# Optimization experiments

Hardware: AMD Instinct MI355X
Metric: run time of the kernel (lower is better)

The kernel has to match this reference:

```python
import jax, jax.numpy as jnp
import numpy as np

B, T, D = 1, 2048, 1024
H = 16
HD = D // H
K = 4
FF = 4 * D
LAYERS = 24
EPS = 1.1920929e-07  # torch.finfo(float32).eps, RMSNorm default


def setup_inputs() -> dict:
    key = jax.random.key(0)
    ks = jax.random.split(key, 16)
    s = 0.02
    return {
        "x": jax.random.normal(ks[0], (B, T, D), jnp.float32),
        "gamma": jax.random.uniform(ks[1], (D,), jnp.float32),
        "beta": jax.random.normal(ks[2], (D,), jnp.float32) * 0.1,
        "iter_scale": jax.random.uniform(ks[3], (1,), jnp.float32),
        "qkv_bases": jax.random.normal(ks[4], (K, 3 * D, D), jnp.float32) * s,
        "o_bases": jax.random.normal(ks[5], (K, D, D), jnp.float32) * s,
        "gate_bases": jax.random.normal(ks[6], (K, FF, D), jnp.float32) * s,
        "up_bases": jax.random.normal(ks[7], (K, FF, D), jnp.float32) * s,
        "down_bases": jax.random.normal(ks[8], (K, D, FF), jnp.float32) * s,
        "alpha_qkv": jax.random.normal(ks[9], (LAYERS, K), jnp.float32) * 0.1 + jnp.eye(LAYERS, K)[:, :K] * 0.0 + jnp.concatenate([jnp.ones((LAYERS, 1)), jnp.zeros((LAYERS, K - 1))], axis=1),
        "alpha_o": jnp.concatenate([jnp.ones((LAYERS, 1)), jnp.zeros((LAYERS, K - 1))], axis=1) + jax.random.normal(ks[10], (LAYERS, K)) * 0.1,
        "alpha_gate": jnp.concatenate([jnp.ones((LAYERS, 1)), jnp.zeros((LAYERS, K - 1))], axis=1) + jax.random.normal(ks[11], (LAYERS, K)) * 0.1,
        "alpha_up": jnp.concatenate([jnp.ones((LAYERS, 1)), jnp.zeros((LAYERS, K - 1))], axis=1) + jax.random.normal(ks[12], (LAYERS, K)) * 0.1,
        "alpha_down": jnp.concatenate([jnp.ones((LAYERS, 1)), jnp.zeros((LAYERS, K - 1))], axis=1) + jax.random.normal(ks[13], (LAYERS, K)) * 0.1,
        "norm1_w": jnp.ones((D,), jnp.float32),
        "norm2_w": jnp.ones((D,), jnp.float32),
        "layer_idx": 5,
    }


def _rmsnorm(x, w):
    return x * jax.lax.rsqrt(jnp.mean(x * x, axis=-1, keepdims=True) + EPS) * w


def reference(x, gamma, beta, iter_scale, qkv_bases, o_bases, gate_bases, up_bases,
              down_bases, alpha_qkv, alpha_o, alpha_gate, alpha_up, alpha_down,
              norm1_w, norm2_w, layer_idx):
    Bx, Tx, Dx = x.shape
    # --- attention sub-block ---
    h = _rmsnorm(x, norm1_w) * gamma + beta
    W_qkv = jnp.einsum('k,kij->ij', alpha_qkv[layer_idx], qkv_bases)  # [3D, D]
    qkv = jnp.einsum('btd,od->bto', h, W_qkv).reshape(Bx, Tx, 3, H, HD)
    qkv = jnp.transpose(qkv, (2, 0, 3, 1, 4))  # [3, B, H, T, HD]
    q, k, v = qkv[0], qkv[1], qkv[2]
    scores = jnp.einsum('bhqd,bhkd->bhqk', q, k) / jnp.sqrt(jnp.asarray(HD, x.dtype))
    causal = jnp.tril(jnp.ones((Tx, Tx), bool))
    scores = jnp.where(causal, scores, jnp.asarray(-jnp.inf, scores.dtype))
    attn = jax.nn.softmax(scores, axis=-1)
    out = jnp.einsum('bhqk,bhkd->bhqd', attn, v)
    out = jnp.transpose(out, (0, 2, 1, 3)).reshape(Bx, Tx, Dx)
    W_o = jnp.einsum('k,kij->ij', alpha_o[layer_idx], o_bases)
    x_attn = x + jnp.einsum('btd,od->bto', out, W_o)
    # --- SwiGLU FFN sub-block ---
    h2 = _rmsnorm(x_attn, norm2_w) * gamma + beta
    W_g = jnp.einsum('k,kij->ij', alpha_gate[layer_idx], gate_bases)
    W_u = jnp.einsum('k,kij->ij', alpha_up[layer_idx], up_bases)
    W_d = jnp.einsum('k,kij->ij', alpha_down[layer_idx], down_bases)
    gate = jnp.einsum('btd,fd->btf', h2, W_g)
    up = jnp.einsum('btd,fd->btf', h2, W_u)
    ffn_out = jnp.einsum('btf,df->btd', jax.nn.silu(gate) * up, W_d)
    block_out = x_attn + ffn_out
    return x + (block_out - x) * iter_scale
```

## Files before the change

### kernel.cpp

```cpp
#include <hip/hip_runtime.h>
#include <hip/hip_bf16.h>
#include <math.h>

typedef __bf16 bf16;
typedef __bf16 bf16x8 __attribute__((ext_vector_type(8)));
typedef __bf16 bf16x4 __attribute__((ext_vector_type(4)));
typedef float f32x4 __attribute__((ext_vector_type(4)));

#define EPSc 1.1920929e-07f
#define LOG2E 1.44269504f

static __device__ __forceinline__ void glds16(const void* g, void* l) {
  __builtin_amdgcn_global_load_lds((const __attribute__((address_space(1))) void*)g,
                                   (__attribute__((address_space(3))) void*)l, 16, 0, 0);
}

static __device__ __forceinline__ bf16x4 comb4(const float* b0, const float* b1,
                                               const float* b2, const float* b3,
                                               float a0, float a1, float a2, float a3) {
  float4 v0 = *(const float4*)b0, v1 = *(const float4*)b1;
  float4 v2 = *(const float4*)b2, v3 = *(const float4*)b3;
  bf16x4 o;
  o[0] = (bf16)(a0*v0.x + a1*v1.x + a2*v2.x + a3*v3.x);
  o[1] = (bf16)(a0*v0.y + a1*v1.y + a2*v2.y + a3*v3.y);
  o[2] = (bf16)(a0*v0.z + a1*v1.z + a2*v2.z + a3*v3.z);
  o[3] = (bf16)(a0*v0.w + a1*v1.w + a2*v2.w + a3*v3.w);
  return o;
}

__global__ __launch_bounds__(256)
void prep1(const float* __restrict__ qkv_b, const float* __restrict__ a_qkv,
           const float* __restrict__ o_b,   const float* __restrict__ a_o,
           const float* __restrict__ x, const float* __restrict__ n1w,
           const float* __restrict__ gamma, const float* __restrict__ beta,
           const int* __restrict__ lidx,
           bf16* __restrict__ Wqkv, bf16* __restrict__ Wo, bf16* __restrict__ hbuf) {
  const int bid = blockIdx.x, tid = threadIdx.x;
  if (bid < 4096) {
    int li = lidx[0];
    const float* base; const float* al; bf16* out; size_t flat, n;
    if (bid < 3072) { base = qkv_b; al = a_qkv; out = Wqkv; flat = (size_t)bid << 10; n = (size_t)3072*1024; }
    else            { base = o_b;   al = a_o;   out = Wo;   flat = (size_t)(bid-3072) << 10; n = (size_t)1024*1024; }
    float a0 = al[li*4], a1 = al[li*4+1], a2 = al[li*4+2], a3 = al[li*4+3];
    size_t off = flat + tid*4;
    bf16x4 o = comb4(base+off, base+n+off, base+2*n+off, base+3*n+off, a0, a1, a2, a3);
    *(bf16x4*)&out[off] = o;
  } else {
    int row = bid - 4096, t = tid;
    const float4* xr = (const float4*)(x + (size_t)row*1024);
    float4 v = xr[t];
    float ss = v.x*v.x + v.y*v.y + v.z*v.z + v.w*v.w;
    #pragma unroll
    for (int off = 32; off > 0; off >>= 1) ss += __shfl_down(ss, off, 64);
    __shared__ float red[4];
    if ((t & 63) == 0) red[t >> 6] = ss;
    __syncthreads();
    float tot = red[0] + red[1] + red[2] + red[3];
    float r = rsqrtf(tot * (1.0f/1024.0f) + EPSc);
    float4 wv = ((const float4*)n1w)[t];
    float4 gv = ((const float4*)gamma)[t];
    float4 bv = ((const float4*)beta)[t];
    bf16x4 o;
    o[0] = (bf16)(v.x*r*wv.x*gv.x + bv.x);
    o[1] = (bf16)(v.y*r*wv.y*gv.y + bv.y);
    o[2] = (bf16)(v.z*r*wv.z*gv.z + bv.z);
    o[3] = (bf16)(v.w*r*wv.w*gv.w + bv.w);
    *(bf16x4*)&hbuf[(size_t)row*1024 + t*4] = o;
  }
}

__global__ __launch_bounds__(256) void rmsnorm_k(const float* __restrict__ x,
                                                 const float* __restrict__ w,
                                                 const float* __restrict__ gamma,
                                                 const float* __restrict__ beta,
                                                 bf16* __restrict__ out) {
  int row = blockIdx.x, t = threadIdx.x;
  const float4* xr = (const float4*)(x + (size_t)row*1024);
  float4 v = xr[t];
  float ss = v.x*v.x + v.y*v.y + v.z*v.z + v.w*v.w;
  #pragma unroll
  for (int off = 32; off > 0; off >>= 1) ss += __shfl_down(ss, off, 64);
  __shared__ float red[4];
  if ((t & 63) == 0) red[t >> 6] = ss;
  __syncthreads();
  float tot = red[0] + red[1] + red[2] + red[3];
  float r = rsqrtf(tot * (1.0f/1024.0f) + EPSc);
  float4 wv = ((const float4*)w)[t];
  float4 gv = ((const float4*)gamma)[t];
  float4 bv = ((const float4*)beta)[t];
  bf16x4 o;
  o[0] = (bf16)(v.x*r*wv.x*gv.x + bv.x);
  o[1] = (bf16)(v.y*r*wv.y*gv.y + bv.y);
  o[2] = (bf16)(v.z*r*wv.z*gv.z + bv.z);
  o[3] = (bf16)(v.w*r*wv.w*gv.w + bv.w);
  *(bf16x4*)&out[(size_t)row*1024 + t*4] = o;
}

template<int EP, int NTW>
__global__ __launch_bounds__(256)
void gemm_bt(const bf16* __restrict__ A, const bf16* __restrict__ Bw,
             int M, int N, int K, int lda, int ldb, int gx,
             float* __restrict__ outf, bf16* __restrict__ outb,
             const float* __restrict__ auxf, const float* __restrict__ auxf2,
             const float* __restrict__ iscale) {
  constexpr int BN = NTW * 32;
  __shared__ __align__(16) bf16 As[2][128*64];
  __shared__ __align__(16) bf16 Bs[2][BN*64];
  const int nwg = gridDim.x;
  const int orig = blockIdx.x;
  const int wg = (orig & 7) * (nwg >> 3) + (orig >> 3);
  const int tn0 = (wg % gx) * BN, tm0 = (wg / gx) * 128;
  const int tid = threadIdx.x, wave = tid >> 6, lane = tid & 63;
  const int lr = lane & 15, lg = lane >> 4;
  const int wr = wave >> 1, wc = wave & 1;
  f32x4 acc[4][NTW] = {};
  const int rs = lane >> 3, cs = (lane & 7) * 8;

  const bf16* Abase = A + (size_t)tm0 * lda;
  const bf16* Bbase = Bw + (size_t)tn0 * ldb;

  auto stage = [&](bf16* as, bf16* bs, int k0) {
    #pragma unroll
    for (int j = 0; j < 4; ++j) {
      int chunk = wave*4 + j;
      int r = chunk*8 + rs;
      glds16(Abase + (size_t)r*lda + k0 + cs, as + chunk*512 + lane*8);
    }
    #pragma unroll
    for (int j = 0; j < NTW; ++j) {
      int chunk = wave*NTW + j;
      int r = chunk*8 + rs;
      glds16(Bbase + (size_t)r*ldb + k0 + cs, bs + chunk*512 + lane*8);
    }
  };
  auto comp = [&](const bf16* as, const bf16* bs) {
    #pragma unroll
    for (int kk = 0; kk < 2; ++kk) {
      bf16x8 av[4], bv[NTW];
      #pragma unroll
      for (int m = 0; m < 4; ++m) av[m] = *(const bf16x8*)&as[(wr*64 + m*16 + lr)*64 + kk*32 + lg*8];
      #pragma unroll
      for (int n = 0; n < NTW; ++n) bv[n] = *(const bf16x8*)&bs[(wc*NTW*16 + n*16 + lr)*64 + kk*32 + lg*8];
      #pragma unroll
      for (int m = 0; m < 4; ++m)
        #pragma unroll
        for (int n = 0; n < NTW; ++n)
          acc[m][n] = __builtin_amdgcn_mfma_f32_16x16x32_bf16(av[m], bv[n], acc[m][n], 0, 0, 0);
    }
  };

  bf16 *a0 = As[0], *a1 = As[1], *b0 = Bs[0], *b1 = Bs[1];
  stage(a0, b0, 0);
  __syncthreads();
  for (int k0 = 64; k0 < K; k0 += 64) {
    stage(a1, b1, k0);
    comp(a0, b0);
    __syncthreads();
    bf16* t;
    t = a0; a0 = a1; a1 = t;
    t = b0; b0 = b1; b1 = t;
  }
  comp(a0, b0);

  float its = 0.f;
  if constexpr (EP == 4) its = iscale[0];

  if constexpr (EP == 5) {
    #pragma unroll
    for (int m = 0; m < 4; ++m)
      #pragma unroll
      for (int j = 0; j < NTW/2; ++j)
        #pragma unroll
        for (int i = 0; i < 4; ++i) {
          int row = tm0 + wr*64 + m*16 + lg*4 + i;
          int col = (tn0 >> 1) + wc*(NTW*8) + j*16 + lr;
          float g = acc[m][2*j][i], u = acc[m][2*j+1][i];
          float s = g / (1.f + __builtin_amdgcn_exp2f(-g * LOG2E));
          outb[(size_t)row * (N >> 1) + col] = (bf16)(s * u);
        }
  } else {
    #pragma unroll
    for (int m = 0; m < 4; ++m)
      #pragma unroll
      for (int n = 0; n < NTW; ++n)
        #pragma unroll
        for (int i = 0; i < 4; ++i) {
          int row = tm0 + wr*64 + m*16 + lg*4 + i;
          int col = tn0 + wc*NTW*16 + n*16 + lr;
          size_t idx = (size_t)row * N + col;
          float v = acc[m][n][i];
          if constexpr (EP == 0) outb[idx] = (bf16)v;
          else if constexpr (EP == 1) outf[idx] = auxf[idx] + v;
          else if constexpr (EP == 4) {
            float xv = auxf[idx], xa = auxf2[idx];
            outf[idx] = xv + (xa + v - xv) * its;
          } else if constexpr (EP == 6) outf[idx] = v;
        }
  }
}

__global__ __launch_bounds__(256)
void reduce2(const float* __restrict__ p0, const float* __restrict__ p1,
             const float* __restrict__ x, const float* __restrict__ xat,
             const float* __restrict__ iscale, float* __restrict__ out) {
  size_t i = (size_t)blockIdx.x * 256 + threadIdx.x;
  float its = iscale[0];
  float4 a = ((const float4*)p0)[i], b = ((const float4*)p1)[i];
  float4 xv = ((const float4*)x)[i], xa = ((const float4*)xat)[i];
  float4 o;
  o.x = xv.x + (xa.x + a.x + b.x - xv.x) * its;
  o.y = xv.y + (xa.y + a.y + b.y - xv.y) * its;
  o.z = xv.z + (xa.z + a.z + b.z - xv.z) * its;
  o.w = xv.w + (xa.w + a.w + b.w - xv.w) * its;
  ((float4*)out)[i] = o;
}

__global__ __launch_bounds__(256)
void attn_mega(const bf16* __restrict__ qkv, bf16* __restrict__ out,
               const float* __restrict__ gate_b, const float* __restrict__ up_b,
               const float* __restrict__ down_b,
               const float* __restrict__ a_gate, const float* __restrict__ a_up,
               const float* __restrict__ a_down, const int* __restrict__ lidx,
               bf16* __restrict__ Wgu, bf16* __restrict__ Wd) {
  __shared__ __align__(16) bf16 Ks[2][64*72];
  __shared__ __align__(16) bf16 Vt[2][64*66];
  __shared__ __align__(16) bf16 Ps[4][16*68];
  const int bid = blockIdx.x;
  const int tid = threadIdx.x;

  if (bid < 256) {
    const int cb = bid;
    int li = lidx[0];
    float g0 = a_gate[li*4], g1 = a_gate[li*4+1], g2 = a_gate[li*4+2], g3 = a_gate[li*4+3];
    float u0 = a_up[li*4],   u1 = a_up[li*4+1],   u2 = a_up[li*4+2],   u3 = a_up[li*4+3];
    float d0 = a_down[li*4], d1 = a_down[li*4+1], d2 = a_down[li*4+2], d3 = a_down[li*4+3];
    const size_t PS = (size_t)4096 * 1024;
    for (int it = 0; it < 48; ++it) {
      int chunk = it * 256 + cb;
      if (chunk < 8192) {
        int r = chunk, w = r & 31;
        int f = ((r >> 5) << 4) + (w & 15);
        const float* base = (w < 16) ? gate_b : up_b;
        float a0 = (w < 16) ? g0 : u0, a1 = (w < 16) ? g1 : u1;
        float a2 = (w < 16) ? g2 : u2, a3 = (w < 16) ? g3 : u3;
        size_t src = (size_t)f*1024 + tid*4;
        bf16x4 o = comb4(base+src, base+PS+src, base+2*PS+src, base+3*PS+src, a0, a1, a2, a3);
        *(bf16x4*)&Wgu[((size_t)r << 10) + tid*4] = o;
      } else {
        size_t off = ((size_t)(chunk - 8192) << 10) + tid*4;
        bf16x4 o = comb4(down_b+off, down_b+PS+off, down_b+2*PS+off, down_b+3*PS+off, d0, d1, d2, d3);
        *(bf16x4*)&Wd[off] = o;
      }
    }
    return;
  }

  const int a = bid - 256;
  const int qb = 31 - (a >> 4);
  const int h = (a & 7) + 8 * ((a >> 3) & 1);
  const int wave = tid >> 6, lane = tid & 63;
  const int lr = lane & 15, lg = lane >> 4;
  const int q0 = qb * 64;

  bf16x8 qf[2];
  {
    const bf16* qrow = qkv + (size_t)(q0 + wave*16 + lr)*3072 + h*64;
    qf[0] = *(const bf16x8*)(qrow + lg*8);
    qf[1] = *(const bf16x8*)(qrow + 32 + lg*8);
  }
  f32x4 o[4] = {};
  float mrow[4], lrow[4];
  #pragma unroll
  for (int i = 0; i < 4; ++i) { mrow[i] = -__builtin_inff(); lrow[i] = 0.f; }

  const int r0 = tid >> 3, r1 = (tid + 256) >> 3;
  const int c0 = (tid & 7) << 3;
  const bf16* kb = qkv + 1024 + h*64 + c0;
  const bf16* vb = qkv + 2048 + h*64 + c0;

  bf16x8 kreg[2], vreg[2];
  auto stage_load = [&](int kv0) {
    kreg[0] = *(const bf16x8*)(kb + (size_t)(kv0 + r0)*3072);
    kreg[1] = *(const bf16x8*)(kb + (size_t)(kv0 + r1)*3072);
    vreg[0] = *(const bf16x8*)(vb + (size_t)(kv0 + r0)*3072);
    vreg[1] = *(const bf16x8*)(vb + (size_t)(kv0 + r1)*3072);
  };
  auto stage_write = [&](int buf) {
    *(bf16x8*)&Ks[buf][r0*72 + c0] = kreg[0];
    *(bf16x8*)&Ks[buf][r1*72 + c0] = kreg[1];
    #pragma unroll
    for (int e = 0; e < 8; ++e) Vt[buf][(c0 + e)*66 + r0] = vreg[0][e];
    #pragma unroll
    for (int e = 0; e < 8; ++e) Vt[buf][(c0 + e)*66 + r1] = vreg[1][e];
  };

  stage_load(0);
  stage_write(0);
  __syncthreads();
  int cur = 0;

  const float C = 0.125f * LOG2E;

  for (int t = 0; t <= qb; ++t) {
    const int kv0 = t * 64;
    if (t < qb) stage_load(kv0 + 64);

    f32x4 s[4] = {};
    __builtin_amdgcn_s_setprio(1);
    #pragma unroll
    for (int n = 0; n < 4; ++n) {
      bf16x8 k0f = *(const bf16x8*)&Ks[cur][(n*16 + lr)*72 + lg*8];
      s[n] = __builtin_amdgcn_mfma_f32_16x16x32_bf16(qf[0], k0f, s[n], 0, 0, 0);
      bf16x8 k1f = *(const bf16x8*)&Ks[cur][(n*16 + lr)*72 + 32 + lg*8];
      s[n] = __builtin_amdgcn_mfma_f32_16x16x32_bf16(qf[1], k1f, s[n], 0, 0, 0);
    }
    __builtin_amdgcn_s_setprio(0);

    if (t == qb) {
      const int qbase = q0 + wave*16 + lg*4;
      #pragma unroll
      for (int n = 0; n < 4; ++n)
        #pragma unroll
        for (int i = 0; i < 4; ++i)
          if (kv0 + n*16 + lr > qbase + i) s[n][i] = -__builtin_inff();
    }

    float mnewr[4], pmn[4];
    #pragma unroll
    for (int i = 0; i < 4; ++i) mnewr[i] = fmaxf(fmaxf(s[0][i], s[1][i]), fmaxf(s[2][i], s[3][i]));
    #pragma unroll
    for (int i = 0; i < 4; ++i)
      #pragma unroll
      for (int off = 1; off < 16; off <<= 1) mnewr[i] = fmaxf(mnewr[i], __shfl_xor(mnewr[i], off, 64));
    bool grow = false;
    #pragma unroll
    for (int i = 0; i < 4; ++i) { pmn[i] = mnewr[i] * C; grow = grow || (pmn[i] > mrow[i] + 8.f); }
    if (__any(grow)) {
      #pragma unroll
      for (int i = 0; i < 4; ++i) {
        float mt = fmaxf(mrow[i], pmn[i]);
        float fc = __builtin_amdgcn_exp2f(mrow[i] - mt);
        mrow[i] = mt;
        lrow[i] *= fc;
        #pragma unroll
        for (int nd = 0; nd < 4; ++nd) o[nd][i] *= fc;
      }
    }
    float rsum[4] = {0.f, 0.f, 0.f, 0.f};
    #pragma unroll
    for (int n = 0; n < 4; ++n)
      #pragma unroll
      for (int i = 0; i < 4; ++i) {
        float e = __builtin_amdgcn_exp2f(__builtin_fmaf(s[n][i], C, -mrow[i]));
        s[n][i] = e;
        rsum[i] += e;
      }
    #pragma unroll
    for (int i = 0; i < 4; ++i)
      #pragma unroll
      for (int off = 1; off < 16; off <<= 1) rsum[i] += __shfl_xor(rsum[i], off, 64);
    #pragma unroll
    for (int i = 0; i < 4; ++i) lrow[i] += rsum[i];
    #pragma unroll
    for (int n = 0; n < 4; ++n)
      #pragma unroll
      for (int i = 0; i < 4; ++i) Ps[wave][(lg*4 + i)*68 + n*16 + lr] = (bf16)s[n][i];
    asm volatile("s_waitcnt lgkmcnt(0)" ::: "memory");
    __builtin_amdgcn_s_setprio(1);
    #pragma unroll
    for (int kk = 0; kk < 2; ++kk) {
      bf16x8 pf = *(const bf16x8*)&Ps[wave][lr*68 + kk*32 + lg*8];
      #pragma unroll
      for (int nd = 0; nd < 4; ++nd) {
        bf16x8 vf = *(const bf16x8*)&Vt[cur][(nd*16 + lr)*66 + kk*32 + lg*8];
        o[nd] = __builtin_amdgcn_mfma_f32_16x16x32_bf16(pf, vf, o[nd], 0, 0, 0);
      }
    }
    __builtin_amdgcn_s_setprio(0);
    if (t < qb) {
      stage_write(cur ^ 1);
      __syncthreads();
      cur ^= 1;
    }
  }
  #pragma unroll
  for (int i = 0; i < 4; ++i) {
    float inv = 1.f / lrow[i];
    #pragma unroll
    for (int nd = 0; nd < 4; ++nd)
      out[(size_t)(q0 + wave*16 + lg*4 + i)*1024 + h*64 + nd*16 + lr] = (bf16)(o[nd][i]*inv);
  }
}

extern "C" void kernel_launch(void* const* d_in, const int* in_sizes, int n_in,
                              void* d_out, int out_size, void* d_ws, size_t ws_size,
                              hipStream_t stream) {
  const float* x        = (const float*)d_in[0];
  const float* gamma    = (const float*)d_in[1];
  const float* beta     = (const float*)d_in[2];
  const float* iscale   = (const float*)d_in[3];
  const float* qkv_b    = (const float*)d_in[4];
  const float* o_b      = (const float*)d_in[5];
  const float* gate_b   = (const float*)d_in[6];
  const float* up_b     = (const float*)d_in[7];
  const float* down_b   = (const float*)d_in[8];
  const float* a_qkv    = (const float*)d_in[9];
  const float* a_o      = (const float*)d_in[10];
  const float* a_gate   = (const float*)d_in[11];
  const float* a_up     = (const float*)d_in[12];
  const float* a_down   = (const float*)d_in[13];
  const float* n1w      = (const float*)d_in[14];
  const float* n2w      = (const float*)d_in[15];
  const int*   lidx     = (const int*)d_in[16];

  char* p = (char*)d_ws;
  auto alloc = [&](size_t bytes) { char* r = p; p += (bytes + 255) & ~(size_t)255; return r; };
  bf16*  Wqkv = (bf16*)alloc((size_t)3072*1024*2);
  bf16*  Wo   = (bf16*)alloc((size_t)1024*1024*2);
  bf16*  Wgu  = (bf16*)alloc((size_t)8192*1024*2);
  bf16*  Wd   = (bf16*)alloc((size_t)1024*4096*2);
  bf16*  hbuf = (bf16*)alloc((size_t)2048*1024*2);
  bf16*  qkvb = (bf16*)alloc((size_t)2048*3072*2);
  bf16*  attn = (bf16*)alloc((size_t)2048*1024*2);
  float* xat  = (float*)alloc((size_t)2048*1024*4);
  bf16*  h2   = (bf16*)alloc((size_t)2048*1024*2);
  bf16*  act  = (bf16*)alloc((size_t)2048*4096*2);
  float* out  = (float*)d_out;
  float* part0 = (float*)Wqkv;
  float* part1 = (float*)qkvb;

  prep1<<<6144, 256, 0, stream>>>(qkv_b, a_qkv, o_b, a_o, x, n1w, gamma, beta, lidx,
                                  Wqkv, Wo, hbuf);
  gemm_bt<0,4><<<24*16, 256, 0, stream>>>(hbuf, Wqkv, 2048, 3072, 1024, 1024, 1024, 24,
                                          nullptr, qkvb, nullptr, nullptr, nullptr);
  attn_mega<<<768, 256, 0, stream>>>(qkvb, attn, gate_b, up_b, down_b,
                                     a_gate, a_up, a_down, lidx, Wgu, Wd);
  gemm_bt<1,2><<<16*16, 256, 0, stream>>>(attn, Wo, 2048, 1024, 1024, 1024, 1024, 16,
                                          xat, nullptr, x, nullptr, nullptr);
  rmsnorm_k<<<2048, 256, 0, stream>>>(xat, n2w, gamma, beta, h2);
  gemm_bt<5,4><<<64*16, 256, 0, stream>>>(h2, Wgu, 2048, 8192, 1024, 1024, 1024, 64,
                                          nullptr, act, nullptr, nullptr, nullptr);
  gemm_bt<6,2><<<16*16, 256, 0, stream>>>(act, Wd, 2048, 1024, 2048, 4096, 4096, 16,
                                          part0, nullptr, nullptr, nullptr, nullptr);
  gemm_bt<6,2><<<16*16, 256, 0, stream>>>(act + 2048, Wd + 2048, 2048, 1024, 2048, 4096, 4096, 16,
                                          part1, nullptr, nullptr, nullptr, nullptr);
  reduce2<<<2048, 256, 0, stream>>>(part0, part1, x, xat, iscale, out);
}
```

Measured before the change: 234.9 us.

## Add 256x256 gate/up GEMM kernel, swizzle LDS, drop split-K down projection

Adds a dedicated 512-thread gate/up GEMM with 256x256 tiles and a finer-grained double-buffered pipeline that interleaves global-to-LDS staging with MFMA phases. It also puts an XOR swizzle on the LDS layout in the generic GEMM to cut bank conflicts. The down projection becomes one full-K GEMM with a fused residual/iter_scale epilogue, which removes the split-K partial buffers and the reduce kernel. The trade-off is that the down projection now runs only 256 workgroups over K=4096, giving less parallelism. The new gate/up kernel also hardcodes its shapes.

```diff
diff --git a/kernel.cpp b/kernel.cpp
--- a/kernel.cpp
+++ b/kernel.cpp
@@ -114,7 +114,10 @@
   const int lr = lane & 15, lg = lane >> 4;
   const int wr = wave >> 1, wc = wave & 1;
   f32x4 acc[4][NTW] = {};
-  const int rs = lane >> 3, cs = (lane & 7) * 8;
+  const int rs = lane >> 3;
+  const int sc = (((lane & 7) ^ rs) << 3);
+  const int x0 = ((lg ^ (lr & 7)) << 3);
+  const int x1 = (((4 + lg) ^ (lr & 7)) << 3);
 
   const bf16* Abase = A + (size_t)tm0 * lda;
   const bf16* Bbase = Bw + (size_t)tn0 * ldb;
@@ -124,23 +127,24 @@
     for (int j = 0; j < 4; ++j) {
       int chunk = wave*4 + j;
       int r = chunk*8 + rs;
-      glds16(Abase + (size_t)r*lda + k0 + cs, as + chunk*512 + lane*8);
+      glds16(Abase + (size_t)r*lda + k0 + sc, as + chunk*512 + lane*8);
     }
     #pragma unroll
     for (int j = 0; j < NTW; ++j) {
       int chunk = wave*NTW + j;
       int r = chunk*8 + rs;
-      glds16(Bbase + (size_t)r*ldb + k0 + cs, bs + chunk*512 + lane*8);
+      glds16(Bbase + (size_t)r*ldb + k0 + sc, bs + chunk*512 + lane*8);
     }
   };
   auto comp = [&](const bf16* as, const bf16* bs) {
     #pragma unroll
     for (int kk = 0; kk < 2; ++kk) {
+      const int x = kk ? x1 : x0;
       bf16x8 av[4], bv[NTW];
       #pragma unroll
-      for (int m = 0; m < 4; ++m) av[m] = *(const bf16x8*)&as[(wr*64 + m*16 + lr)*64 + kk*32 + lg*8];
-      #pragma unroll
-      for (int n = 0; n < NTW; ++n) bv[n] = *(const bf16x8*)&bs[(wc*NTW*16 + n*16 + lr)*64 + kk*32 + lg*8];
+      for (int m = 0; m < 4; ++m) av[m] = *(const bf16x8*)&as[(wr*64 + m*16 + lr)*64 + x];
+      #pragma unroll
+      for (int n = 0; n < NTW; ++n) bv[n] = *(const bf16x8*)&bs[(wc*NTW*16 + n*16 + lr)*64 + x];
       #pragma unroll
       for (int m = 0; m < 4; ++m)
         #pragma unroll
@@ -164,55 +168,117 @@
 
   float its = 0.f;
   if constexpr (EP == 4) its = iscale[0];
-
-  if constexpr (EP == 5) {
-    #pragma unroll
-    for (int m = 0; m < 4; ++m)
-      #pragma unroll
-      for (int j = 0; j < NTW/2; ++j)
+  #pragma unroll
+  for (int m = 0; m < 4; ++m)
+    #pragma unroll
+    for (int n = 0; n < NTW; ++n)
+      #pragma unroll
+      for (int i = 0; i < 4; ++i) {
+        int row = tm0 + wr*64 + m*16 + lg*4 + i;
+        int col = tn0 + wc*NTW*16 + n*16 + lr;
+        size_t idx = (size_t)row * N + col;
+        float v = acc[m][n][i];
+        if constexpr (EP == 0) outb[idx] = (bf16)v;
+        else if constexpr (EP == 1) outf[idx] = auxf[idx] + v;
+        else if constexpr (EP == 4) {
+          float xv = auxf[idx], xa = auxf2[idx];
+          outf[idx] = xv + (xa + v - xv) * its;
+        }
+      }
+}
+
+__global__ __launch_bounds__(512, 2)
+void gemm_gu256(const bf16* __restrict__ A, const bf16* __restrict__ Bw,
+                bf16* __restrict__ outb) {
+  __shared__ __align__(16) bf16 L[2][2][2][8192];
+  const int orig = blockIdx.x;
+  const int wg = (orig & 7) * 32 + (orig >> 3);
+  const int tn0 = (wg & 31) * 256, tm0 = (wg >> 5) * 256;
+  const int tid = threadIdx.x, wave = tid >> 6, lane = tid & 63;
+  const int lr = lane & 15, lg = lane >> 4;
+  const int wr = wave >> 2, wn = wave & 3;
+  const int rs8 = lane >> 3;
+  const int gc8 = (((lane & 7) ^ rs8) << 3);
+  const int xk0 = ((lg ^ (lr & 7)) << 3);
+  const int xk1 = (((4 + lg) ^ (lr & 7)) << 3);
+  f32x4 acc[8][4] = {};
+
+  const bf16* Ab = A + (size_t)tm0 * 1024;
+  const bf16* Bb = Bw + (size_t)tn0 * 1024;
+
+  auto stage_half = [&](bf16* dst, const bf16* gbase, int half, int k0) {
+    #pragma unroll
+    for (int l = 0; l < 2; ++l) {
+      int r = half*128 + (wave*2 + l)*8 + rs8;
+      glds16(gbase + (size_t)r*1024 + k0 + gc8, dst + (wave*2 + l)*512 + lane*8);
+    }
+  };
+
+  stage_half(&L[0][0][0][0], Ab, 0, 0);
+  stage_half(&L[0][0][1][0], Ab, 1, 0);
+  stage_half(&L[0][1][0][0], Bb, 0, 0);
+  stage_half(&L[0][1][1][0], Bb, 1, 0);
+  stage_half(&L[1][1][0][0], Bb, 0, 64);
+  stage_half(&L[1][1][1][0], Bb, 1, 64);
+  asm volatile("s_waitcnt vmcnt(4)" ::: "memory");
+  __builtin_amdgcn_s_barrier();
+
+  for (int t = 0; t < 16; ++t) {
+    const int b = t & 1;
+    const bf16* ah = &L[b][0][wr][0];
+    const bf16* bh = &L[b][1][wn >> 1][0];
+    bf16x8 breg[4][2];
+    #pragma unroll
+    for (int p = 0; p < 4; ++p) {
+      if (p == 0) {
         #pragma unroll
-        for (int i = 0; i < 4; ++i) {
-          int row = tm0 + wr*64 + m*16 + lg*4 + i;
-          int col = (tn0 >> 1) + wc*(NTW*8) + j*16 + lr;
-          float g = acc[m][2*j][i], u = acc[m][2*j+1][i];
-          float s = g / (1.f + __builtin_amdgcn_exp2f(-g * LOG2E));
-          outb[(size_t)row * (N >> 1) + col] = (bf16)(s * u);
+        for (int n = 0; n < 4; ++n) {
+          int row = (wn & 1)*64 + n*16 + lr;
+          breg[n][0] = *(const bf16x8*)&bh[row*64 + xk0];
+          breg[n][1] = *(const bf16x8*)&bh[row*64 + xk1];
         }
-  } else {
-    #pragma unroll
-    for (int m = 0; m < 4; ++m)
-      #pragma unroll
-      for (int n = 0; n < NTW; ++n)
+      }
+      bf16x8 av[2][2];
+      #pragma unroll
+      for (int mi = 0; mi < 2; ++mi) {
+        int row = p*32 + mi*16 + lr;
+        av[mi][0] = *(const bf16x8*)&ah[row*64 + xk0];
+        av[mi][1] = *(const bf16x8*)&ah[row*64 + xk1];
+      }
+      if (p == 0 && t < 15) stage_half(&L[b^1][0][0][0], Ab, 0, (t+1)*64);
+      if (p == 1 && t < 15) stage_half(&L[b^1][0][1][0], Ab, 1, (t+1)*64);
+      if (p == 2 && t < 14) stage_half(&L[b][1][0][0], Bb, 0, (t+2)*64);
+      if (p == 3 && t < 14) stage_half(&L[b][1][1][0], Bb, 1, (t+2)*64);
+      __builtin_amdgcn_s_barrier();
+      __builtin_amdgcn_s_setprio(1);
+      #pragma unroll
+      for (int mi = 0; mi < 2; ++mi)
         #pragma unroll
-        for (int i = 0; i < 4; ++i) {
-          int row = tm0 + wr*64 + m*16 + lg*4 + i;
-          int col = tn0 + wc*NTW*16 + n*16 + lr;
-          size_t idx = (size_t)row * N + col;
-          float v = acc[m][n][i];
-          if constexpr (EP == 0) outb[idx] = (bf16)v;
-          else if constexpr (EP == 1) outf[idx] = auxf[idx] + v;
-          else if constexpr (EP == 4) {
-            float xv = auxf[idx], xa = auxf2[idx];
-            outf[idx] = xv + (xa + v - xv) * its;
-          } else if constexpr (EP == 6) outf[idx] = v;
+        for (int n = 0; n < 4; ++n) {
+          acc[p*2+mi][n] = __builtin_amdgcn_mfma_f32_16x16x32_bf16(av[mi][0], breg[n][0], acc[p*2+mi][n], 0, 0, 0);
+          acc[p*2+mi][n] = __builtin_amdgcn_mfma_f32_16x16x32_bf16(av[mi][1], breg[n][1], acc[p*2+mi][n], 0, 0, 0);
         }
-  }
-}
-
-__global__ __launch_bounds__(256)
-void reduce2(const float* __restrict__ p0, const float* __restrict__ p1,
-             const float* __restrict__ x, const float* __restrict__ xat,
-             const float* __restrict__ iscale, float* __restrict__ out) {
-  size_t i = (size_t)blockIdx.x * 256 + threadIdx.x;
-  float its = iscale[0];
-  float4 a = ((const float4*)p0)[i], b = ((const float4*)p1)[i];
-  float4 xv = ((const float4*)x)[i], xa = ((const float4*)xat)[i];
-  float4 o;
-  o.x = xv.x + (xa.x + a.x + b.x - xv.x) * its;
-  o.y = xv.y + (xa.y + a.y + b.y - xv.y) * its;
-  o.z = xv.z + (xa.z + a.z + b.z - xv.z) * its;
-  o.w = xv.w + (xa.w + a.w + b.w - xv.w) * its;
-  ((float4*)out)[i] = o;
+      __builtin_amdgcn_s_setprio(0);
+      if (p == 3) {
+        if (t >= 14) asm volatile("s_waitcnt vmcnt(0)" ::: "memory");
+        else         asm volatile("s_waitcnt vmcnt(4)" ::: "memory");
+      }
+      __builtin_amdgcn_s_barrier();
+    }
+  }
+
+  #pragma unroll
+  for (int mf = 0; mf < 8; ++mf)
+    #pragma unroll
+    for (int j = 0; j < 2; ++j)
+      #pragma unroll
+      for (int i = 0; i < 4; ++i) {
+        int row = tm0 + wr*128 + mf*16 + lg*4 + i;
+        int col = (tn0 >> 1) + wn*32 + j*16 + lr;
+        float g = acc[mf][2*j][i], u = acc[mf][2*j+1][i];
+        float s = g / (1.f + __builtin_amdgcn_exp2f(-g * LOG2E));
+        outb[(size_t)row * 4096 + col] = (bf16)(s * u);
+      }
 }
 
 __global__ __launch_bounds__(256)
@@ -426,8 +492,6 @@
   bf16*  h2   = (bf16*)alloc((size_t)2048*1024*2);
   bf16*  act  = (bf16*)alloc((size_t)2048*4096*2);
   float* out  = (float*)d_out;
-  float* part0 = (float*)Wqkv;
-  float* part1 = (float*)qkvb;
 
   prep1<<<6144, 256, 0, stream>>>(qkv_b, a_qkv, o_b, a_o, x, n1w, gamma, beta, lidx,
                                   Wqkv, Wo, hbuf);
@@ -438,11 +502,7 @@
   gemm_bt<1,2><<<16*16, 256, 0, stream>>>(attn, Wo, 2048, 1024, 1024, 1024, 1024, 16,
                                           xat, nullptr, x, nullptr, nullptr);
   rmsnorm_k<<<2048, 256, 0, stream>>>(xat, n2w, gamma, beta, h2);
-  gemm_bt<5,4><<<64*16, 256, 0, stream>>>(h2, Wgu, 2048, 8192, 1024, 1024, 1024, 64,
-                                          nullptr, act, nullptr, nullptr, nullptr);
-  gemm_bt<6,2><<<16*16, 256, 0, stream>>>(act, Wd, 2048, 1024, 2048, 4096, 4096, 16,
-                                          part0, nullptr, nullptr, nullptr, nullptr);
-  gemm_bt<6,2><<<16*16, 256, 0, stream>>>(act + 2048, Wd + 2048, 2048, 1024, 2048, 4096, 4096, 16,
-                                          part1, nullptr, nullptr, nullptr, nullptr);
-  reduce2<<<2048, 256, 0, stream>>>(part0, part1, x, xat, iscale, out);
-}
+  gemm_gu256<<<256, 512, 0, stream>>>(h2, Wgu, act);
+  gemm_bt<4,2><<<16*16, 256, 0, stream>>>(act, Wd, 2048, 1024, 4096, 4096, 4096, 16,
+                                          out, nullptr, x, xat, iscale);
+}
```

Result: faster. 204.0 us (-13.2%).
